# Optimization experiments

Measured on AMD Instinct MI355X. Metric: run time of the kernel, lower is better.

The kernel has to match this reference:

```python
import jax, jax.numpy as jnp
import numpy as np

N = 100000  # nodes per answer graph
E = 3200000  # edges per answer graph
D = 300  # GloVe embedding dim
H = 16  # hidden dim


def gcn_conv(x, src, dst, W, b):
    """PyG-style GCNConv: add self-loops, symmetric norm, aggregate at target."""
    n = x.shape[0]
    loops = jnp.arange(n, dtype=src.dtype)
    s = jnp.concatenate([src, loops])  # [E+N]
    d = jnp.concatenate([dst, loops])
    deg = jnp.zeros((n,), x.dtype).at[d].add(1.0)
    dis = jnp.where(deg > 0, jax.lax.rsqrt(deg), 0.0)  # deg^{-1/2}
    h = x @ W  # [N, out]
    norm = dis[s] * dis[d]  # [E+N]
    msg = h[s] * norm[:, None]
    agg = jax.ops.segment_sum(msg, d, num_segments=n)
    return agg + b


def _one_answer(x, ei, W1, b1, W2, b2):
    src, dst = ei[0], ei[1]
    h = jax.nn.relu(gcn_conv(x, src, dst, W1, b1))
    # dropout omitted (eval mode: F.dropout(training=False) is identity)
    out = gcn_conv(h, src, dst, W2, b2)  # [N, 1]
    return out.mean()


def setup_inputs() -> dict:
    key = jax.random.key(0)
    k1, k2, k3, k4 = jax.random.split(key, 4)
    emb = jax.random.normal(k1, (5, N, D), jnp.float32)
    edge_index = jax.random.randint(k2, (5, 2, E), 0, N, jnp.int64)
    W1 = jax.random.normal(k3, (D, H), jnp.float32) * (1.0 / np.sqrt(D))
    b1 = jnp.zeros((H,), jnp.float32)
    W2 = jax.random.normal(k4, (H, 1), jnp.float32) * (1.0 / np.sqrt(H))
    b2 = jnp.zeros((1,), jnp.float32)
    return {"emb": emb, "edge_index": edge_index, "W1": W1, "b1": b1, "W2": W2, "b2": b2}


def reference(emb, edge_index, W1, b1, W2, b2):
    scores = jax.vmap(_one_answer, in_axes=(0, 0, None, None, None, None))(
        emb, edge_index, W1, b1, W2, b2)  # [5]
    return jax.nn.softmax(scores, axis=0)
```

## Files before the change

kernel.cpp:

```cpp
#include <hip/hip_runtime.h>
#include <hip/hip_bf16.h>

#define N_ 100000
#define E_ 3200000
#define DIM 300
#define HID 16
#define NGRAPH 5
#define NB 196
#define BSH 9
#define BNODES 512
#define CAP 20480
#define SCAP 24576

__device__ __forceinline__ void fatomic(float* p, float v) { unsafeAtomicAdd(p, v); }

__global__ __launch_bounds__(256) void bucket_kernel(const int* __restrict__ ei,
                                                     unsigned* __restrict__ bcur,
                                                     unsigned* __restrict__ bedge) {
    int g = blockIdx.y;
    const int4* src4 = (const int4*)(ei + (size_t)g * 2 * E_);
    const int4* dst4 = (const int4*)(ei + (size_t)g * 2 * E_ + E_);
    unsigned* bc = bcur + (size_t)g * NB;
    unsigned* be = bedge + (size_t)g * NB * CAP;
    __shared__ unsigned hist[NB], curs[NB];
    int tid = threadIdx.x;
    const int CHUNK = 4096;
    const int nchunk = (E_ + CHUNK - 1) / CHUNK;
    for (int c = blockIdx.x; c < nchunk; c += gridDim.x) {
        int cb = c * CHUNK;
        for (int i = tid; i < NB; i += 256) hist[i] = 0u;
        __syncthreads();
        int4 sv[4], dv[4]; bool val[4];
#pragma unroll
        for (int k = 0; k < 4; ++k) {
            int e0 = cb + k * 1024 + tid * 4;
            val[k] = (e0 < E_);
            if (val[k]) { sv[k] = src4[e0 >> 2]; dv[k] = dst4[e0 >> 2]; }
        }
#pragma unroll
        for (int k = 0; k < 4; ++k) if (val[k]) {
            atomicAdd(&hist[((unsigned)dv[k].x) >> BSH], 1u);
            atomicAdd(&hist[((unsigned)dv[k].y) >> BSH], 1u);
            atomicAdd(&hist[((unsigned)dv[k].z) >> BSH], 1u);
            atomicAdd(&hist[((unsigned)dv[k].w) >> BSH], 1u);
        }
        __syncthreads();
        for (int i = tid; i < NB; i += 256) curs[i] = atomicAdd(&bc[i], hist[i]);
        __syncthreads();
#define EMIT(S, D) { unsigned bb = ((unsigned)(D)) >> BSH; \
        unsigned pos = atomicAdd(&curs[bb], 1u); \
        if (pos < CAP) be[(size_t)bb * CAP + pos] = (((unsigned)(S)) << BSH) | (((unsigned)(D)) & (BNODES - 1)); }
#pragma unroll
        for (int k = 0; k < 4; ++k) if (val[k]) {
            EMIT(sv[k].x, dv[k].x)
            EMIT(sv[k].y, dv[k].y)
            EMIT(sv[k].z, dv[k].z)
            EMIT(sv[k].w, dv[k].w)
        }
#undef EMIT
        __syncthreads();
    }
}

__global__ __launch_bounds__(256) void sortb_kernel(const unsigned* __restrict__ bcur,
                                                    const unsigned* __restrict__ bedge,
                                                    unsigned* __restrict__ ssrc,
                                                    unsigned* __restrict__ offA,
                                                    unsigned* __restrict__ degA,
                                                    float* __restrict__ dis) {
    int g = blockIdx.y, b = blockIdx.x;
    __shared__ unsigned hist[BNODES], offL[BNODES], curL[BNODES], part[256];
    int tid = threadIdx.x;
    hist[tid] = 0u; hist[tid + 256] = 0u;
    __syncthreads();
    unsigned n = bcur[(size_t)g * NB + b]; if (n > CAP) n = CAP;
    const unsigned* beb = bedge + ((size_t)g * NB + b) * CAP;
    for (unsigned i = tid; i < n; i += 256) atomicAdd(&hist[beb[i] & (BNODES - 1)], 1u);
    __syncthreads();
    unsigned d0 = hist[2 * tid], d1 = hist[2 * tid + 1];
    unsigned p0 = (d0 + 7u) & ~7u, p1 = (d1 + 7u) & ~7u;
    part[tid] = p0 + p1;
    __syncthreads();
    for (int o = 1; o < 256; o <<= 1) {
        unsigned v = (tid >= o) ? part[tid - o] : 0u;
        __syncthreads();
        part[tid] += v;
        __syncthreads();
    }
    unsigned base = part[tid] - p0 - p1;
    offL[2 * tid] = base;     curL[2 * tid] = base;
    offL[2 * tid + 1] = base + p0; curL[2 * tid + 1] = base + p0;
    int node0 = b << BSH;
    unsigned sbase = (unsigned)(((size_t)g * NB + b) * SCAP);
    float* disg = dis + (size_t)g * N_;
    unsigned* offg = offA + (size_t)g * (NB << BSH);
    unsigned* degg = degA + (size_t)g * (NB << BSH);
    {
        int i = 2 * tid, node = node0 + i;
        offg[node] = sbase + offL[i]; degg[node] = d0;
        if (node < N_) disg[node] = rsqrtf((float)d0 + 1.0f);
        i = 2 * tid + 1; node = node0 + i;
        offg[node] = sbase + offL[i]; degg[node] = d1;
        if (node < N_) disg[node] = rsqrtf((float)d1 + 1.0f);
    }
    __syncthreads();
    for (unsigned i = tid; i < n; i += 256) {
        unsigned pk = beb[i];
        unsigned pos = atomicAdd(&curL[pk & (BNODES - 1)], 1u);
        ssrc[(size_t)sbase + pos] = pk >> BSH;
    }
}

#define FMA4(acc, sv, wv) \
    acc.x += (sv) * (wv).x; acc.y += (sv) * (wv).y; acc.z += (sv) * (wv).z; acc.w += (sv) * (wv).w;

__global__ __launch_bounds__(256) void gemm_kernel(const float* __restrict__ x,
                                                   const float* __restrict__ W1,
                                                   const float* __restrict__ dis,
                                                   float* __restrict__ hd, int ntot) {
    __shared__ float wsh[DIM * HID];
    for (int i = threadIdx.x; i < DIM * HID; i += blockDim.x) wsh[i] = W1[i];
    __syncthreads();
    int node = blockIdx.x * blockDim.x + threadIdx.x;
    if (node >= ntot) return;
    const float4* xr = (const float4*)(x + (size_t)node * DIM);
    float4 a0 = {0,0,0,0}, a1 = {0,0,0,0}, a2 = {0,0,0,0}, a3 = {0,0,0,0};
    float4 q0, q1, q2, q3;
#define STEP(XS, B) \
    q0 = wr[(B)+0]; q1 = wr[(B)+1]; q2 = wr[(B)+2]; q3 = wr[(B)+3]; \
    FMA4(a0, XS, q0) FMA4(a1, XS, q1) FMA4(a2, XS, q2) FMA4(a3, XS, q3)
#pragma unroll 3
    for (int k4 = 0; k4 < DIM / 4; ++k4) {
        float4 xv = xr[k4];
        const float4* wr = (const float4*)(wsh + k4 * 4 * HID);
        STEP(xv.x, 0)
        STEP(xv.y, 4)
        STEP(xv.z, 8)
        STEP(xv.w, 12)
    }
#undef STEP
    float dn = dis[node];
    a0.x *= dn; a0.y *= dn; a0.z *= dn; a0.w *= dn;
    a1.x *= dn; a1.y *= dn; a1.z *= dn; a1.w *= dn;
    a2.x *= dn; a2.y *= dn; a2.z *= dn; a2.w *= dn;
    a3.x *= dn; a3.y *= dn; a3.z *= dn; a3.w *= dn;
    float4* hr = (float4*)(hd + (size_t)node * HID);
    hr[0] = a0; hr[1] = a1; hr[2] = a2; hr[3] = a3;
}

__global__ __launch_bounds__(512) void bagg_kernel(const unsigned* __restrict__ ssrc,
                                                   const unsigned* __restrict__ offA,
                                                   const unsigned* __restrict__ degA,
                                                   const float* __restrict__ hd,
                                                   const float* __restrict__ dis,
                                                   const float* __restrict__ b1,
                                                   const float* __restrict__ W2,
                                                   float* __restrict__ t_) {
    int g = blockIdx.y, b = blockIdx.x;
    const float* hdg = hd + (size_t)g * N_ * HID;
    const float* disg = dis + (size_t)g * N_;
    const unsigned* offg = offA + (size_t)g * (NB << BSH);
    const unsigned* degg = degA + (size_t)g * (NB << BSH);
    float* tg = t_ + (size_t)g * N_;
    int tid = threadIdx.x, j = tid & 15, sub = tid >> 4;
    float b1j = b1[j], w2j = W2[j];
    int node0 = b << BSH;
#pragma unroll 1
    for (int m = 0; m < 16; ++m) {
        int node = node0 + sub + (m << 5);
        if (node >= N_) continue;
        unsigned k0 = offg[node], dg = degg[node];
        float acc = hdg[(size_t)node * HID + j];
        unsigned k = 0;
        for (; k + 8 <= dg; k += 8) {
            const int4* ip = (const int4*)(ssrc + k0 + k);
            int4 i0 = ip[0], i1 = ip[1];
            float v0 = hdg[(size_t)(unsigned)i0.x * HID + j];
            float v1 = hdg[(size_t)(unsigned)i0.y * HID + j];
            float v2 = hdg[(size_t)(unsigned)i0.z * HID + j];
            float v3 = hdg[(size_t)(unsigned)i0.w * HID + j];
            float v4 = hdg[(size_t)(unsigned)i1.x * HID + j];
            float v5 = hdg[(size_t)(unsigned)i1.y * HID + j];
            float v6 = hdg[(size_t)(unsigned)i1.z * HID + j];
            float v7 = hdg[(size_t)(unsigned)i1.w * HID + j];
            acc += ((v0 + v1) + (v2 + v3)) + ((v4 + v5) + (v6 + v7));
        }
        for (; k < dg; ++k) acc += hdg[(size_t)ssrc[k0 + k] * HID + j];
        float dn = disg[node];
        float val = fmaxf(acc * dn + b1j, 0.f) * w2j;
        val += __shfl_xor(val, 1);
        val += __shfl_xor(val, 2);
        val += __shfl_xor(val, 4);
        val += __shfl_xor(val, 8);
        if (j == 0) tg[node] = val * dn;
    }
}

__global__ __launch_bounds__(512) void score2_kernel(const unsigned* __restrict__ ssrc,
                                                     const unsigned* __restrict__ offA,
                                                     const unsigned* __restrict__ degA,
                                                     const float* __restrict__ t_,
                                                     const float* __restrict__ dis,
                                                     float* __restrict__ S) {
    int g = blockIdx.y, b = blockIdx.x;
    const float* tg = t_ + (size_t)g * N_;
    const float* disg = dis + (size_t)g * N_;
    const unsigned* offg = offA + (size_t)g * (NB << BSH);
    const unsigned* degg = degA + (size_t)g * (NB << BSH);
    int tid = threadIdx.x, j = tid & 3, grp = tid >> 2;
    int node0 = b << BSH;
    float c = 0.f;
#pragma unroll 1
    for (int m = 0; m < 4; ++m) {
        int node = node0 + grp + (m << 7);
        if (node >= N_) continue;
        unsigned k0 = offg[node], dg = degg[node];
        float acc = 0.f;
        for (unsigned k = j; k < dg; k += 4) acc += tg[ssrc[k0 + k]];
        acc += __shfl_xor(acc, 1);
        acc += __shfl_xor(acc, 2);
        if (j == 0) c += disg[node] * (acc + tg[node]);
    }
    for (int o = 32; o > 0; o >>= 1) c += __shfl_down(c, o);
    __shared__ float red[8];
    int wid = tid >> 6, lane = tid & 63;
    if (lane == 0) red[wid] = c;
    __syncthreads();
    if (tid == 0) {
        float s = 0.f;
        for (int w = 0; w < 8; ++w) s += red[w];
        fatomic(&S[g], s);
    }
}

__global__ void final_kernel(const float* __restrict__ S, const float* __restrict__ b2,
                             float* __restrict__ out) {
    if (threadIdx.x == 0) {
        float sc[NGRAPH];
        float m = -1e30f;
        for (int g = 0; g < NGRAPH; ++g) {
            sc[g] = b2[0] + S[g] * (1.0f / N_);
            m = fmaxf(m, sc[g]);
        }
        float sum = 0.f;
        for (int g = 0; g < NGRAPH; ++g) { sc[g] = expf(sc[g] - m); sum += sc[g]; }
        for (int g = 0; g < NGRAPH; ++g) out[g] = sc[g] / sum;
    }
}

extern "C" void kernel_launch(void* const* d_in, const int* in_sizes, int n_in,
                              void* d_out, int out_size, void* d_ws, size_t ws_size,
                              hipStream_t stream) {
    const float* emb = (const float*)d_in[0];
    const int* ei    = (const int*)d_in[1];
    const float* W1  = (const float*)d_in[2];
    const float* b1  = (const float*)d_in[3];
    const float* W2  = (const float*)d_in[4];
    const float* b2  = (const float*)d_in[5];
    float* out = (float*)d_out;

    float* S = (float*)d_ws;
    unsigned* bcurAll = (unsigned*)((char*)d_ws + 256);
    size_t hdr = 256 + (size_t)NGRAPH * NB * 4;
    hdr = (hdr + 255) & ~(size_t)255;
    char* base = (char*)d_ws + hdr;
    size_t avail = (ws_size > hdr) ? ws_size - hdr : 0;

    size_t sz_be   = (size_t)NB * CAP * 4;
    size_t sz_ss   = (size_t)NB * SCAP * 4;
    size_t sz_off  = (size_t)(NB << BSH) * 4;
    size_t sz_hd   = (size_t)N_ * HID * 4;
    size_t sz_dis  = (size_t)N_ * 4;
    size_t sz_t    = (size_t)N_ * 4;
    size_t per = sz_be + sz_ss + 2 * sz_off + sz_hd + sz_dis + sz_t + 1024;
    int maxChunk = (int)(avail / per);
    if (maxChunk > NGRAPH) maxChunk = NGRAPH;
    if (maxChunk < 1) maxChunk = 1;

    hipMemsetAsync(d_ws, 0, 256 + (size_t)NGRAPH * NB * 4, stream);

    for (int g0 = 0; g0 < NGRAPH; g0 += maxChunk) {
        int ng = (NGRAPH - g0 < maxChunk) ? (NGRAPH - g0) : maxChunk;
        char* p = base;
        unsigned* bedge = (unsigned*)p; p += (size_t)ng * sz_be;
        unsigned* ssrc  = (unsigned*)p; p += (size_t)ng * sz_ss;
        unsigned* offA  = (unsigned*)p; p += (size_t)ng * sz_off;
        unsigned* degA  = (unsigned*)p; p += (size_t)ng * sz_off;
        float* hd  = (float*)p; p += (size_t)ng * sz_hd;
        float* dis = (float*)p; p += (size_t)ng * sz_dis;
        float* t_  = (float*)p;
        unsigned* bcur = bcurAll + (size_t)g0 * NB;

        const int* eic  = ei  + (size_t)g0 * 2 * E_;
        const float* xc = emb + (size_t)g0 * N_ * DIM;

        bucket_kernel<<<dim3(128, ng), 256, 0, stream>>>(eic, bcur, bedge);
        sortb_kernel<<<dim3(NB, ng), 256, 0, stream>>>(bcur, bedge, ssrc, offA, degA, dis);
        gemm_kernel<<<dim3((ng * N_ + 255) / 256), 256, 0, stream>>>(xc, W1, dis, hd, ng * N_);
        bagg_kernel<<<dim3(NB, ng), 512, 0, stream>>>(ssrc, offA, degA, hd, dis, b1, W2, t_);
        score2_kernel<<<dim3(NB, ng), 512, 0, stream>>>(ssrc, offA, degA, t_, dis, S + g0);
    }
    final_kernel<<<1, 64, 0, stream>>>(S, b2, out);
}
```

Measured before the change: 884.3 us.

## Pad adjacency lists with dummy node, two nodes per thread in GEMM, larger bucket chunks

Adjacency lists are padded to multiples of eight with a sentinel index pointing at an extra zeroed row in hd and t, so the aggregation loops need no scalar tail. The GEMM now computes two nodes per thread so each shared-memory W1 load is reused twice. The bucket kernel uses larger chunks with a re-read of src/dst in a strided loop and more blocks. The padding adds extra gathers of the zero row, and the larger GEMM per-thread footprint raises register pressure.

Result: slower. 1.208 ms (+36.5%).

```diff
diff --git a/kernel.cpp b/kernel.cpp
--- a/kernel.cpp
+++ b/kernel.cpp
@@ -11,6 +11,7 @@
 #define BNODES 512
 #define CAP 20480
 #define SCAP 24576
+#define NPAD (N_ + 8)
 
 __device__ __forceinline__ void fatomic(float* p, float v) { unsafeAtomicAdd(p, v); }
 
@@ -24,25 +25,19 @@
     unsigned* be = bedge + (size_t)g * NB * CAP;
     __shared__ unsigned hist[NB], curs[NB];
     int tid = threadIdx.x;
-    const int CHUNK = 4096;
+    const int CHUNK = 16384;
     const int nchunk = (E_ + CHUNK - 1) / CHUNK;
     for (int c = blockIdx.x; c < nchunk; c += gridDim.x) {
-        int cb = c * CHUNK;
+        int q0 = c * (CHUNK / 4);
+        int q1 = q0 + (CHUNK / 4) < (E_ / 4) ? q0 + (CHUNK / 4) : (E_ / 4);
         for (int i = tid; i < NB; i += 256) hist[i] = 0u;
         __syncthreads();
-        int4 sv[4], dv[4]; bool val[4];
-#pragma unroll
-        for (int k = 0; k < 4; ++k) {
-            int e0 = cb + k * 1024 + tid * 4;
-            val[k] = (e0 < E_);
-            if (val[k]) { sv[k] = src4[e0 >> 2]; dv[k] = dst4[e0 >> 2]; }
-        }
-#pragma unroll
-        for (int k = 0; k < 4; ++k) if (val[k]) {
-            atomicAdd(&hist[((unsigned)dv[k].x) >> BSH], 1u);
-            atomicAdd(&hist[((unsigned)dv[k].y) >> BSH], 1u);
-            atomicAdd(&hist[((unsigned)dv[k].z) >> BSH], 1u);
-            atomicAdd(&hist[((unsigned)dv[k].w) >> BSH], 1u);
+        for (int e4 = q0 + tid; e4 < q1; e4 += 256) {
+            int4 dv = dst4[e4];
+            atomicAdd(&hist[((unsigned)dv.x) >> BSH], 1u);
+            atomicAdd(&hist[((unsigned)dv.y) >> BSH], 1u);
+            atomicAdd(&hist[((unsigned)dv.z) >> BSH], 1u);
+            atomicAdd(&hist[((unsigned)dv.w) >> BSH], 1u);
         }
         __syncthreads();
         for (int i = tid; i < NB; i += 256) curs[i] = atomicAdd(&bc[i], hist[i]);
@@ -50,12 +45,13 @@
 #define EMIT(S, D) { unsigned bb = ((unsigned)(D)) >> BSH; \
         unsigned pos = atomicAdd(&curs[bb], 1u); \
         if (pos < CAP) be[(size_t)bb * CAP + pos] = (((unsigned)(S)) << BSH) | (((unsigned)(D)) & (BNODES - 1)); }
-#pragma unroll
-        for (int k = 0; k < 4; ++k) if (val[k]) {
-            EMIT(sv[k].x, dv[k].x)
-            EMIT(sv[k].y, dv[k].y)
-            EMIT(sv[k].z, dv[k].z)
-            EMIT(sv[k].w, dv[k].w)
+        for (int e4 = q0 + tid; e4 < q1; e4 += 256) {
+            int4 sv = src4[e4];
+            int4 dv = dst4[e4];
+            EMIT(sv.x, dv.x)
+            EMIT(sv.y, dv.y)
+            EMIT(sv.z, dv.z)
+            EMIT(sv.w, dv.w)
         }
 #undef EMIT
         __syncthreads();
@@ -88,7 +84,7 @@
         __syncthreads();
     }
     unsigned base = part[tid] - p0 - p1;
-    offL[2 * tid] = base;     curL[2 * tid] = base;
+    offL[2 * tid] = base;         curL[2 * tid] = base;
     offL[2 * tid + 1] = base + p0; curL[2 * tid + 1] = base + p0;
     int node0 = b << BSH;
     unsigned sbase = (unsigned)(((size_t)g * NB + b) * SCAP);
@@ -99,9 +95,11 @@
         int i = 2 * tid, node = node0 + i;
         offg[node] = sbase + offL[i]; degg[node] = d0;
         if (node < N_) disg[node] = rsqrtf((float)d0 + 1.0f);
+        for (unsigned k = d0; k < p0; ++k) ssrc[(size_t)sbase + offL[i] + k] = (unsigned)N_;
         i = 2 * tid + 1; node = node0 + i;
         offg[node] = sbase + offL[i]; degg[node] = d1;
         if (node < N_) disg[node] = rsqrtf((float)d1 + 1.0f);
+        for (unsigned k = d1; k < p1; ++k) ssrc[(size_t)sbase + offL[i] + k] = (unsigned)N_;
     }
     __syncthreads();
     for (unsigned i = tid; i < n; i += 256) {
@@ -117,35 +115,60 @@
 __global__ __launch_bounds__(256) void gemm_kernel(const float* __restrict__ x,
                                                    const float* __restrict__ W1,
                                                    const float* __restrict__ dis,
-                                                   float* __restrict__ hd, int ntot) {
+                                                   float* __restrict__ hd, int ngr) {
     __shared__ float wsh[DIM * HID];
     for (int i = threadIdx.x; i < DIM * HID; i += blockDim.x) wsh[i] = W1[i];
-    __syncthreads();
-    int node = blockIdx.x * blockDim.x + threadIdx.x;
-    if (node >= ntot) return;
-    const float4* xr = (const float4*)(x + (size_t)node * DIM);
+    if (blockIdx.x == 0 && threadIdx.x < ngr) {
+        float4* pz = (float4*)(hd + ((size_t)threadIdx.x * NPAD + N_) * HID);
+        float4 z = {0.f, 0.f, 0.f, 0.f};
+        pz[0] = z; pz[1] = z; pz[2] = z; pz[3] = z;
+    }
+    __syncthreads();
+    int ntot = ngr * N_;
+    int n0 = blockIdx.x * 512 + threadIdx.x;
+    int n1 = n0 + 256;
+    bool v1 = (n1 < ntot);
+    if (n0 >= ntot) return;
+    const float4* xr0 = (const float4*)(x + (size_t)n0 * DIM);
+    const float4* xr1 = (const float4*)(x + (size_t)n1 * DIM);
     float4 a0 = {0,0,0,0}, a1 = {0,0,0,0}, a2 = {0,0,0,0}, a3 = {0,0,0,0};
+    float4 c0 = {0,0,0,0}, c1 = {0,0,0,0}, c2 = {0,0,0,0}, c3 = {0,0,0,0};
     float4 q0, q1, q2, q3;
-#define STEP(XS, B) \
+#define STEP2(XS, YS, B) \
     q0 = wr[(B)+0]; q1 = wr[(B)+1]; q2 = wr[(B)+2]; q3 = wr[(B)+3]; \
-    FMA4(a0, XS, q0) FMA4(a1, XS, q1) FMA4(a2, XS, q2) FMA4(a3, XS, q3)
+    FMA4(a0, XS, q0) FMA4(a1, XS, q1) FMA4(a2, XS, q2) FMA4(a3, XS, q3) \
+    FMA4(c0, YS, q0) FMA4(c1, YS, q1) FMA4(c2, YS, q2) FMA4(c3, YS, q3)
 #pragma unroll 3
     for (int k4 = 0; k4 < DIM / 4; ++k4) {
-        float4 xv = xr[k4];
+        float4 xv = xr0[k4];
+        float4 yv = v1 ? xr1[k4] : xv;
         const float4* wr = (const float4*)(wsh + k4 * 4 * HID);
-        STEP(xv.x, 0)
-        STEP(xv.y, 4)
-        STEP(xv.z, 8)
-        STEP(xv.w, 12)
-    }
-#undef STEP
-    float dn = dis[node];
-    a0.x *= dn; a0.y *= dn; a0.z *= dn; a0.w *= dn;
-    a1.x *= dn; a1.y *= dn; a1.z *= dn; a1.w *= dn;
-    a2.x *= dn; a2.y *= dn; a2.z *= dn; a2.w *= dn;
-    a3.x *= dn; a3.y *= dn; a3.z *= dn; a3.w *= dn;
-    float4* hr = (float4*)(hd + (size_t)node * HID);
-    hr[0] = a0; hr[1] = a1; hr[2] = a2; hr[3] = a3;
+        STEP2(xv.x, yv.x, 0)
+        STEP2(xv.y, yv.y, 4)
+        STEP2(xv.z, yv.z, 8)
+        STEP2(xv.w, yv.w, 12)
+    }
+#undef STEP2
+    {
+        float dn = dis[n0];
+        a0.x *= dn; a0.y *= dn; a0.z *= dn; a0.w *= dn;
+        a1.x *= dn; a1.y *= dn; a1.z *= dn; a1.w *= dn;
+        a2.x *= dn; a2.y *= dn; a2.z *= dn; a2.w *= dn;
+        a3.x *= dn; a3.y *= dn; a3.z *= dn; a3.w *= dn;
+        int gi = n0 / N_, local = n0 - gi * N_;
+        float4* hr = (float4*)(hd + ((size_t)gi * NPAD + local) * HID);
+        hr[0] = a0; hr[1] = a1; hr[2] = a2; hr[3] = a3;
+    }
+    if (v1) {
+        float dn = dis[n1];
+        c0.x *= dn; c0.y *= dn; c0.z *= dn; c0.w *= dn;
+        c1.x *= dn; c1.y *= dn; c1.z *= dn; c1.w *= dn;
+        c2.x *= dn; c2.y *= dn; c2.z *= dn; c2.w *= dn;
+        c3.x *= dn; c3.y *= dn; c3.z *= dn; c3.w *= dn;
+        int gi = n1 / N_, local = n1 - gi * N_;
+        float4* hr = (float4*)(hd + ((size_t)gi * NPAD + local) * HID);
+        hr[0] = c0; hr[1] = c1; hr[2] = c2; hr[3] = c3;
+    }
 }
 
 __global__ __launch_bounds__(512) void bagg_kernel(const unsigned* __restrict__ ssrc,
@@ -157,12 +180,13 @@
                                                    const float* __restrict__ W2,
                                                    float* __restrict__ t_) {
     int g = blockIdx.y, b = blockIdx.x;
-    const float* hdg = hd + (size_t)g * N_ * HID;
+    const float* hdg = hd + (size_t)g * NPAD * HID;
     const float* disg = dis + (size_t)g * N_;
     const unsigned* offg = offA + (size_t)g * (NB << BSH);
     const unsigned* degg = degA + (size_t)g * (NB << BSH);
-    float* tg = t_ + (size_t)g * N_;
+    float* tg = t_ + (size_t)g * NPAD;
     int tid = threadIdx.x, j = tid & 15, sub = tid >> 4;
+    if (b == 0 && tid == 0) tg[N_] = 0.f;
     float b1j = b1[j], w2j = W2[j];
     int node0 = b << BSH;
 #pragma unroll 1
@@ -170,9 +194,9 @@
         int node = node0 + sub + (m << 5);
         if (node >= N_) continue;
         unsigned k0 = offg[node], dg = degg[node];
+        unsigned dgp = (dg + 7u) & ~7u;
         float acc = hdg[(size_t)node * HID + j];
-        unsigned k = 0;
-        for (; k + 8 <= dg; k += 8) {
+        for (unsigned k = 0; k < dgp; k += 8) {
             const int4* ip = (const int4*)(ssrc + k0 + k);
             int4 i0 = ip[0], i1 = ip[1];
             float v0 = hdg[(size_t)(unsigned)i0.x * HID + j];
@@ -185,7 +209,6 @@
             float v7 = hdg[(size_t)(unsigned)i1.w * HID + j];
             acc += ((v0 + v1) + (v2 + v3)) + ((v4 + v5) + (v6 + v7));
         }
-        for (; k < dg; ++k) acc += hdg[(size_t)ssrc[k0 + k] * HID + j];
         float dn = disg[node];
         float val = fmaxf(acc * dn + b1j, 0.f) * w2j;
         val += __shfl_xor(val, 1);
@@ -203,7 +226,7 @@
                                                      const float* __restrict__ dis,
                                                      float* __restrict__ S) {
     int g = blockIdx.y, b = blockIdx.x;
-    const float* tg = t_ + (size_t)g * N_;
+    const float* tg = t_ + (size_t)g * NPAD;
     const float* disg = dis + (size_t)g * N_;
     const unsigned* offg = offA + (size_t)g * (NB << BSH);
     const unsigned* degg = degA + (size_t)g * (NB << BSH);
@@ -215,8 +238,9 @@
         int node = node0 + grp + (m << 7);
         if (node >= N_) continue;
         unsigned k0 = offg[node], dg = degg[node];
+        unsigned dgp = (dg + 7u) & ~7u;
         float acc = 0.f;
-        for (unsigned k = j; k < dg; k += 4) acc += tg[ssrc[k0 + k]];
+        for (unsigned k = j; k < dgp; k += 4) acc += tg[ssrc[k0 + k]];
         acc += __shfl_xor(acc, 1);
         acc += __shfl_xor(acc, 2);
         if (j == 0) c += disg[node] * (acc + tg[node]);
@@ -269,9 +293,9 @@
     size_t sz_be   = (size_t)NB * CAP * 4;
     size_t sz_ss   = (size_t)NB * SCAP * 4;
     size_t sz_off  = (size_t)(NB << BSH) * 4;
-    size_t sz_hd   = (size_t)N_ * HID * 4;
+    size_t sz_hd   = (size_t)NPAD * HID * 4;
     size_t sz_dis  = (size_t)N_ * 4;
-    size_t sz_t    = (size_t)N_ * 4;
+    size_t sz_t    = (size_t)NPAD * 4;
     size_t per = sz_be + sz_ss + 2 * sz_off + sz_hd + sz_dis + sz_t + 1024;
     int maxChunk = (int)(avail / per);
     if (maxChunk > NGRAPH) maxChunk = NGRAPH;
@@ -294,9 +318,9 @@
         const int* eic  = ei  + (size_t)g0 * 2 * E_;
         const float* xc = emb + (size_t)g0 * N_ * DIM;
 
-        bucket_kernel<<<dim3(128, ng), 256, 0, stream>>>(eic, bcur, bedge);
+        bucket_kernel<<<dim3(196, ng), 256, 0, stream>>>(eic, bcur, bedge);
         sortb_kernel<<<dim3(NB, ng), 256, 0, stream>>>(bcur, bedge, ssrc, offA, degA, dis);
-        gemm_kernel<<<dim3((ng * N_ + 255) / 256), 256, 0, stream>>>(xc, W1, dis, hd, ng * N_);
+        gemm_kernel<<<dim3((ng * N_ + 511) / 512), 256, 0, stream>>>(xc, W1, dis, hd, ng);
         bagg_kernel<<<dim3(NB, ng), 512, 0, stream>>>(ssrc, offA, degA, hd, dis, b1, W2, t_);
         score2_kernel<<<dim3(NB, ng), 512, 0, stream>>>(ssrc, offA, degA, t_, dis, S + g0);
     }
```

## Pad adjacency lists with zero sentinel node and stage GEMM input through LDS

Applied to the files above, without the earlier changes.

Each node's neighbor list is padded to a multiple of 8 with a sentinel index pointing at an added zero row in hd and a zero entry in t_. This removes the scalar tail loops in the two aggregation kernels, and bagg gains a 16-wide unrolled gather. The GEMM now loads x through shared memory in coalesced 20-column chunks instead of per-thread strided float4 rows. The sentinel rows and padded strides (NPAD) add some extra writes and layout complexity, and padded entries do wasted gathers.

After: 1.156 ms. +30.7%, slower.

```diff
diff --git a/kernel.cpp b/kernel.cpp
--- a/kernel.cpp
+++ b/kernel.cpp
@@ -11,6 +11,7 @@
 #define BNODES 512
 #define CAP 20480
 #define SCAP 24576
+#define NPAD (N_ + 8)
 
 __device__ __forceinline__ void fatomic(float* p, float v) { unsafeAtomicAdd(p, v); }
 
@@ -88,7 +89,7 @@
         __syncthreads();
     }
     unsigned base = part[tid] - p0 - p1;
-    offL[2 * tid] = base;     curL[2 * tid] = base;
+    offL[2 * tid] = base;         curL[2 * tid] = base;
     offL[2 * tid + 1] = base + p0; curL[2 * tid + 1] = base + p0;
     int node0 = b << BSH;
     unsigned sbase = (unsigned)(((size_t)g * NB + b) * SCAP);
@@ -99,9 +100,11 @@
         int i = 2 * tid, node = node0 + i;
         offg[node] = sbase + offL[i]; degg[node] = d0;
         if (node < N_) disg[node] = rsqrtf((float)d0 + 1.0f);
+        for (unsigned k = d0; k < p0; ++k) ssrc[(size_t)sbase + offL[i] + k] = (unsigned)N_;
         i = 2 * tid + 1; node = node0 + i;
         offg[node] = sbase + offL[i]; degg[node] = d1;
         if (node < N_) disg[node] = rsqrtf((float)d1 + 1.0f);
+        for (unsigned k = d1; k < p1; ++k) ssrc[(size_t)sbase + offL[i] + k] = (unsigned)N_;
     }
     __syncthreads();
     for (unsigned i = tid; i < n; i += 256) {
@@ -111,41 +114,57 @@
     }
 }
 
-#define FMA4(acc, sv, wv) \
-    acc.x += (sv) * (wv).x; acc.y += (sv) * (wv).y; acc.z += (sv) * (wv).z; acc.w += (sv) * (wv).w;
-
+#define CCH 20
 __global__ __launch_bounds__(256) void gemm_kernel(const float* __restrict__ x,
                                                    const float* __restrict__ W1,
                                                    const float* __restrict__ dis,
-                                                   float* __restrict__ hd, int ntot) {
+                                                   float* __restrict__ hd, int ngr) {
     __shared__ float wsh[DIM * HID];
-    for (int i = threadIdx.x; i < DIM * HID; i += blockDim.x) wsh[i] = W1[i];
-    __syncthreads();
-    int node = blockIdx.x * blockDim.x + threadIdx.x;
-    if (node >= ntot) return;
-    const float4* xr = (const float4*)(x + (size_t)node * DIM);
+    __shared__ float xt[256 * (CCH + 1)];
+    int tid = threadIdx.x;
+    for (int i = tid; i < DIM * HID; i += 256) wsh[i] = W1[i];
+    if (blockIdx.x == 0 && tid < ngr) {
+        float4* pz = (float4*)(hd + ((size_t)tid * NPAD + N_) * HID);
+        float4 z = {0.f, 0.f, 0.f, 0.f};
+        pz[0] = z; pz[1] = z; pz[2] = z; pz[3] = z;
+    }
+    int ntot = ngr * N_;
+    int node0 = blockIdx.x * 256;
+    int node = node0 + tid;
     float4 a0 = {0,0,0,0}, a1 = {0,0,0,0}, a2 = {0,0,0,0}, a3 = {0,0,0,0};
-    float4 q0, q1, q2, q3;
-#define STEP(XS, B) \
-    q0 = wr[(B)+0]; q1 = wr[(B)+1]; q2 = wr[(B)+2]; q3 = wr[(B)+3]; \
-    FMA4(a0, XS, q0) FMA4(a1, XS, q1) FMA4(a2, XS, q2) FMA4(a3, XS, q3)
-#pragma unroll 3
-    for (int k4 = 0; k4 < DIM / 4; ++k4) {
-        float4 xv = xr[k4];
-        const float4* wr = (const float4*)(wsh + k4 * 4 * HID);
-        STEP(xv.x, 0)
-        STEP(xv.y, 4)
-        STEP(xv.z, 8)
-        STEP(xv.w, 12)
-    }
-#undef STEP
-    float dn = dis[node];
-    a0.x *= dn; a0.y *= dn; a0.z *= dn; a0.w *= dn;
-    a1.x *= dn; a1.y *= dn; a1.z *= dn; a1.w *= dn;
-    a2.x *= dn; a2.y *= dn; a2.z *= dn; a2.w *= dn;
-    a3.x *= dn; a3.y *= dn; a3.z *= dn; a3.w *= dn;
-    float4* hr = (float4*)(hd + (size_t)node * HID);
-    hr[0] = a0; hr[1] = a1; hr[2] = a2; hr[3] = a3;
+#pragma unroll 1
+    for (int c = 0; c < DIM / CCH; ++c) {
+        __syncthreads();
+#pragma unroll
+        for (int it = 0; it < CCH; ++it) {
+            int i = tid + it * 256;
+            int row = i / CCH, col = i - row * CCH;
+            int nd = node0 + row;
+            xt[row * (CCH + 1) + col] = (nd < ntot) ? x[(size_t)nd * DIM + c * CCH + col] : 0.f;
+        }
+        __syncthreads();
+        const float* xr = xt + tid * (CCH + 1);
+#pragma unroll
+        for (int k = 0; k < CCH; ++k) {
+            float xs = xr[k];
+            const float4* wr = (const float4*)(wsh + (c * CCH + k) * HID);
+            float4 q0 = wr[0], q1 = wr[1], q2 = wr[2], q3 = wr[3];
+            a0.x += xs * q0.x; a0.y += xs * q0.y; a0.z += xs * q0.z; a0.w += xs * q0.w;
+            a1.x += xs * q1.x; a1.y += xs * q1.y; a1.z += xs * q1.z; a1.w += xs * q1.w;
+            a2.x += xs * q2.x; a2.y += xs * q2.y; a2.z += xs * q2.z; a2.w += xs * q2.w;
+            a3.x += xs * q3.x; a3.y += xs * q3.y; a3.z += xs * q3.z; a3.w += xs * q3.w;
+        }
+    }
+    if (node < ntot) {
+        float dn = dis[node];
+        a0.x *= dn; a0.y *= dn; a0.z *= dn; a0.w *= dn;
+        a1.x *= dn; a1.y *= dn; a1.z *= dn; a1.w *= dn;
+        a2.x *= dn; a2.y *= dn; a2.z *= dn; a2.w *= dn;
+        a3.x *= dn; a3.y *= dn; a3.z *= dn; a3.w *= dn;
+        int gi = node / N_, local = node - gi * N_;
+        float4* hr = (float4*)(hd + ((size_t)gi * NPAD + local) * HID);
+        hr[0] = a0; hr[1] = a1; hr[2] = a2; hr[3] = a3;
+    }
 }
 
 __global__ __launch_bounds__(512) void bagg_kernel(const unsigned* __restrict__ ssrc,
@@ -157,12 +176,13 @@
                                                    const float* __restrict__ W2,
                                                    float* __restrict__ t_) {
     int g = blockIdx.y, b = blockIdx.x;
-    const float* hdg = hd + (size_t)g * N_ * HID;
+    const float* hdg = hd + (size_t)g * NPAD * HID;
     const float* disg = dis + (size_t)g * N_;
     const unsigned* offg = offA + (size_t)g * (NB << BSH);
     const unsigned* degg = degA + (size_t)g * (NB << BSH);
-    float* tg = t_ + (size_t)g * N_;
+    float* tg = t_ + (size_t)g * NPAD;
     int tid = threadIdx.x, j = tid & 15, sub = tid >> 4;
+    if (b == 0 && tid == 0) tg[N_] = 0.f;
     float b1j = b1[j], w2j = W2[j];
     int node0 = b << BSH;
 #pragma unroll 1
@@ -170,9 +190,32 @@
         int node = node0 + sub + (m << 5);
         if (node >= N_) continue;
         unsigned k0 = offg[node], dg = degg[node];
+        unsigned dgp = (dg + 7u) & ~7u;
         float acc = hdg[(size_t)node * HID + j];
         unsigned k = 0;
-        for (; k + 8 <= dg; k += 8) {
+        for (; k + 16 <= dgp; k += 16) {
+            const int4* ip = (const int4*)(ssrc + k0 + k);
+            int4 i0 = ip[0], i1 = ip[1], i2 = ip[2], i3 = ip[3];
+            float v0 = hdg[(size_t)(unsigned)i0.x * HID + j];
+            float v1 = hdg[(size_t)(unsigned)i0.y * HID + j];
+            float v2 = hdg[(size_t)(unsigned)i0.z * HID + j];
+            float v3 = hdg[(size_t)(unsigned)i0.w * HID + j];
+            float v4 = hdg[(size_t)(unsigned)i1.x * HID + j];
+            float v5 = hdg[(size_t)(unsigned)i1.y * HID + j];
+            float v6 = hdg[(size_t)(unsigned)i1.z * HID + j];
+            float v7 = hdg[(size_t)(unsigned)i1.w * HID + j];
+            float v8 = hdg[(size_t)(unsigned)i2.x * HID + j];
+            float v9 = hdg[(size_t)(unsigned)i2.y * HID + j];
+            float va = hdg[(size_t)(unsigned)i2.z * HID + j];
+            float vb = hdg[(size_t)(unsigned)i2.w * HID + j];
+            float vc = hdg[(size_t)(unsigned)i3.x * HID + j];
+            float vd = hdg[(size_t)(unsigned)i3.y * HID + j];
+            float ve = hdg[(size_t)(unsigned)i3.z * HID + j];
+            float vf = hdg[(size_t)(unsigned)i3.w * HID + j];
+            acc += (((v0 + v1) + (v2 + v3)) + ((v4 + v5) + (v6 + v7)))
+                 + (((v8 + v9) + (va + vb)) + ((vc + vd) + (ve + vf)));
+        }
+        for (; k < dgp; k += 8) {
             const int4* ip = (const int4*)(ssrc + k0 + k);
             int4 i0 = ip[0], i1 = ip[1];
             float v0 = hdg[(size_t)(unsigned)i0.x * HID + j];
@@ -185,7 +228,6 @@
             float v7 = hdg[(size_t)(unsigned)i1.w * HID + j];
             acc += ((v0 + v1) + (v2 + v3)) + ((v4 + v5) + (v6 + v7));
         }
-        for (; k < dg; ++k) acc += hdg[(size_t)ssrc[k0 + k] * HID + j];
         float dn = disg[node];
         float val = fmaxf(acc * dn + b1j, 0.f) * w2j;
         val += __shfl_xor(val, 1);
@@ -203,7 +245,7 @@
                                                      const float* __restrict__ dis,
                                                      float* __restrict__ S) {
     int g = blockIdx.y, b = blockIdx.x;
-    const float* tg = t_ + (size_t)g * N_;
+    const float* tg = t_ + (size_t)g * NPAD;
     const float* disg = dis + (size_t)g * N_;
     const unsigned* offg = offA + (size_t)g * (NB << BSH);
     const unsigned* degg = degA + (size_t)g * (NB << BSH);
@@ -215,8 +257,9 @@
         int node = node0 + grp + (m << 7);
         if (node >= N_) continue;
         unsigned k0 = offg[node], dg = degg[node];
+        unsigned dgp = (dg + 7u) & ~7u;
         float acc = 0.f;
-        for (unsigned k = j; k < dg; k += 4) acc += tg[ssrc[k0 + k]];
+        for (unsigned k = j; k < dgp; k += 4) acc += tg[ssrc[k0 + k]];
         acc += __shfl_xor(acc, 1);
         acc += __shfl_xor(acc, 2);
         if (j == 0) c += disg[node] * (acc + tg[node]);
@@ -269,9 +312,9 @@
     size_t sz_be   = (size_t)NB * CAP * 4;
     size_t sz_ss   = (size_t)NB * SCAP * 4;
     size_t sz_off  = (size_t)(NB << BSH) * 4;
-    size_t sz_hd   = (size_t)N_ * HID * 4;
+    size_t sz_hd   = (size_t)NPAD * HID * 4;
     size_t sz_dis  = (size_t)N_ * 4;
-    size_t sz_t    = (size_t)N_ * 4;
+    size_t sz_t    = (size_t)NPAD * 4;
     size_t per = sz_be + sz_ss + 2 * sz_off + sz_hd + sz_dis + sz_t + 1024;
     int maxChunk = (int)(avail / per);
     if (maxChunk > NGRAPH) maxChunk = NGRAPH;
@@ -296,7 +339,7 @@
 
         bucket_kernel<<<dim3(128, ng), 256, 0, stream>>>(eic, bcur, bedge);
         sortb_kernel<<<dim3(NB, ng), 256, 0, stream>>>(bcur, bedge, ssrc, offA, degA, dis);
-        gemm_kernel<<<dim3((ng * N_ + 255) / 256), 256, 0, stream>>>(xc, W1, dis, hd, ng * N_);
+        gemm_kernel<<<dim3((ng * N_ + 255) / 256), 256, 0, stream>>>(xc, W1, dis, hd, ng);
         bagg_kernel<<<dim3(NB, ng), 512, 0, stream>>>(ssrc, offA, degA, hd, dis, b1, W2, t_);
         score2_kernel<<<dim3(NB, ng), 512, 0, stream>>>(ssrc, offA, degA, t_, dis, S + g0);
     }
```
